# Kernel tuning notes

Hardware: AMD Instinct MI355X
Metric: run time of the kernel (lower is better)

The kernel has to match this reference:

```python
import jax, jax.numpy as jnp
import numpy as np

COST_CLASS, COST_BBOX, COST_GIOU = 1.0, 5.0, 2.0


def _box_area(b):
    return (b[..., 2] - b[..., 0]) * (b[..., 3] - b[..., 1])


def _generalized_box_iou(b1, b2):
    # b1: (B,Q,4), b2: (B,N,4), xyxy -> (B,Q,N)
    a1 = _box_area(b1)[:, :, None]
    a2 = _box_area(b2)[:, None, :]
    lt = jnp.maximum(b1[:, :, None, :2], b2[:, None, :, :2])
    rb = jnp.minimum(b1[:, :, None, 2:], b2[:, None, :, 2:])
    wh = jnp.clip(rb - lt, 0.0)
    inter = wh[..., 0] * wh[..., 1]
    union = a1 + a2 - inter
    iou = inter / union
    lt_c = jnp.minimum(b1[:, :, None, :2], b2[:, None, :, :2])
    rb_c = jnp.maximum(b1[:, :, None, 2:], b2[:, None, :, 2:])
    wh_c = jnp.clip(rb_c - lt_c, 0.0)
    area_c = wh_c[..., 0] * wh_c[..., 1]
    return iou - (area_c - union) / area_c


@jax.jit
def _cost_matrix(pred_logits, pred_boxes, tgt_labels, tgt_boxes):
    B, Q, _ = pred_logits.shape
    N = tgt_labels.shape[1]
    out_prob = jax.nn.softmax(pred_logits, axis=-1)  # (B,Q,C+1)
    idx = jnp.broadcast_to(tgt_labels[:, None, :], (B, Q, N))
    cost_class = -jnp.take_along_axis(out_prob, idx, axis=-1)          # (B,Q,N)
    cost_bbox = jnp.abs(pred_boxes[:, :, None, :] - tgt_boxes[:, None, :, :]).sum(-1)  # L1 cdist
    cost_giou = -_generalized_box_iou(pred_boxes, tgt_boxes)
    return COST_CLASS * cost_class + COST_BBOX * cost_bbox + COST_GIOU * cost_giou


def _lsa(cost):
    """Shortest-augmenting-path Hungarian (Jonker-Volgenant style).
    cost: (n, m) with n <= m. Returns col4row[i] = assigned column of row i.
    Matches scipy.optimize.linear_sum_assignment (minimization)."""
    n, m = cost.shape
    INF = np.inf
    u = np.zeros(n + 1)
    v = np.zeros(m + 1)
    p = np.zeros(m + 1, dtype=np.int64)   # p[j] = row (1-indexed) assigned to col j
    way = np.zeros(m + 1, dtype=np.int64)
    for i in range(1, n + 1):
        p[0] = i
        j0 = 0
        minv = np.full(m + 1, INF)
        used = np.zeros(m + 1, dtype=bool)
        while True:
            used[j0] = True
            i0 = p[j0]
            cur = cost[i0 - 1] - u[i0] - v[1:]
            free = ~used[1:]
            upd = free & (cur < minv[1:])
            minv[1:][upd] = cur[upd]
            way[1:][upd] = j0
            cand = np.where(free, minv[1:], INF)
            j1 = int(np.argmin(cand)) + 1
            delta = cand[j1 - 1]
            uj = np.nonzero(used)[0]
            u[p[uj]] += delta
            v[uj] -= delta
            minv[~used] -= delta
            j0 = j1
            if p[j0] == 0:
                break
        while j0 != 0:
            j1 = way[j0]
            p[j0] = p[j1]
            j0 = j1
    col4row = np.zeros(n, dtype=np.int64)
    for j in range(1, m + 1):
        if p[j] != 0:
            col4row[p[j] - 1] = j - 1
    return col4row


def setup_inputs() -> dict:
    key = jax.random.key(0)
    k1, k2, k3, k4, k5 = jax.random.split(key, 5)
    B, Q, N, C1 = 64, 600, 80, 92

    def make_boxes(kx, ky, shape):
        xy = jax.random.uniform(kx, shape + (2,)) * 0.6
        wh = jax.random.uniform(ky, shape + (2,)) * 0.35 + 0.02
        return jnp.concatenate([xy, xy + wh], axis=-1)  # valid xyxy

    pred_logits = jax.random.normal(k1, (B, Q, C1), dtype=jnp.float32)
    pred_boxes = make_boxes(k2, k3, (B, Q))
    tgt_labels = jax.random.randint(k4, (B, N), 0, 91)
    tgt_boxes = make_boxes(k5, jax.random.fold_in(k5, 1), (B, N))
    return {"pred_logits": pred_logits, "pred_boxes": pred_boxes,
            "tgt_labels": tgt_labels, "tgt_boxes": tgt_boxes}


def reference(pred_logits, pred_boxes, tgt_labels, tgt_boxes):
    # Batched cost-matrix build on device, then host Hungarian per sample
    # (mirrors the original's .cpu().numpy() + scipy linear_sum_assignment).
    C = np.asarray(_cost_matrix(pred_logits, pred_boxes, tgt_labels, tgt_boxes))  # (B,Q,N)
    B, Q, N = C.shape
    rows = np.empty((B, N), dtype=np.int64)
    cols = np.empty((B, N), dtype=np.int64)
    for b in range(B):
        q_of_t = _lsa(C[b].T)              # transpose: N <= Q; query index per target
        order = np.argsort(q_of_t, kind="stable")
        rows[b] = q_of_t[order]            # sorted query (row) indices
        cols[b] = order                    # matching target (col) indices
    return jnp.asarray(rows), jnp.asarray(cols)
```

## Files before the change

### kernel.cpp

```cpp
#include <hip/hip_runtime.h>
#include <math.h>

#define BB 64
#define QQ 600
#define NT 80
#define NC 92
#define SLOTS 10
#define NTILE 10
#define NTHR 256
#define NWAVE 4
#define MAXROUNDS 48
#define SPINCAP (1 << 20)

__global__ __launch_bounds__(256) void matcher_kernel(
    const float* __restrict__ logits,
    const float* __restrict__ pboxes,
    const int*   __restrict__ tlabels,
    const float* __restrict__ tboxes,
    float* __restrict__ cost,
    float* __restrict__ pm1,
    float* __restrict__ pm2,
    int*   __restrict__ pmj,
    int*   __restrict__ done,
    int* __restrict__ rows_out,
    int* __restrict__ cols_out)
{
    __shared__ float tile[64 * 93];
    __shared__ float s_m[64], s_s[64];
    __shared__ float s_pm[4 * 64], s_ps[4 * 64];
    __shared__ float s_tb[NT * 4];
    __shared__ int   s_tl[NT];
    __shared__ double vA[QQ];
    __shared__ double u[NT];
    __shared__ double bidm1[NT], bidm2[NT];
    __shared__ int    bidj[NT], bidver[NT];
    __shared__ int    pA[QQ];
    __shared__ int    verA[QQ];
    __shared__ int    colrow[QQ];
    __shared__ int    assigned[NT];
    __shared__ int    plist[NT];
    __shared__ int    pcnt;
    __shared__ int    wayA[QQ];
    __shared__ int    c4r[NT];
    __shared__ int    djkA[NT];

    const int g   = blockIdx.x;
    const int b   = g / NTILE;
    const int tix = g % NTILE;
    const int tid = threadIdx.x;
    const int qq  = tid & 63;
    const int wv  = tid >> 6;
    const float* C = cost + (size_t)b * NT * QQ;

    {
        const int q0 = tix * 64;
        const int nq = min(64, QQ - q0);
        const float* src = logits + ((size_t)b * QQ + q0) * NC;
        for (int idx = tid; idx < nq * NC; idx += 256) {
            const int r = idx / NC;
            tile[r * 93 + (idx - r * NC)] = src[idx];
        }
        for (int i = tid; i < NT * 4; i += 256) s_tb[i] = tboxes[b * NT * 4 + i];
        for (int i = tid; i < NT;     i += 256) s_tl[i] = tlabels[b * NT + i];
        __syncthreads();

        if (tid < nq) {
            const float* r = &tile[tid * 93];
            float m0 = r[0], m1 = r[1], m2 = r[2], m3 = r[3];
            for (int c = 4; c < NC; c += 4) {
                m0 = fmaxf(m0, r[c]);   m1 = fmaxf(m1, r[c+1]);
                m2 = fmaxf(m2, r[c+2]); m3 = fmaxf(m3, r[c+3]);
            }
            const float m = fmaxf(fmaxf(m0, m1), fmaxf(m2, m3));
            float s0 = 0.f, s1 = 0.f, s2 = 0.f, s3 = 0.f;
            for (int c = 0; c < NC; c += 4) {
                s0 += expf(r[c]   - m); s1 += expf(r[c+1] - m);
                s2 += expf(r[c+2] - m); s3 += expf(r[c+3] - m);
            }
            s_m[tid] = m; s_s[tid] = (s0 + s1) + (s2 + s3);
        }
        __syncthreads();

        const bool valid = qq < nq;
        float px1 = 0.f, py1 = 0.f, px2 = 0.f, py2 = 0.f, pa = 0.f, m = 0.f, s = 1.f;
        if (valid) {
            const float* pb = pboxes + ((size_t)b * QQ + q0 + qq) * 4;
            px1 = pb[0]; py1 = pb[1]; px2 = pb[2]; py2 = pb[3];
            pa  = (px2 - px1) * (py2 - py1);
            m = s_m[qq]; s = s_s[qq];
        }
        float* crow = cost + (size_t)b * NT * QQ + q0 + qq;
        const int q = q0 + qq;

        for (int tt = 0; tt < 20; ++tt) {
            const int t = wv * 20 + tt;
            float costv = INFINITY;
            if (valid) {
                const int lbl = s_tl[t];
                const float cc = -(expf(tile[qq * 93 + lbl] - m) / s);
                const float tx1 = s_tb[t*4+0], ty1 = s_tb[t*4+1];
                const float tx2 = s_tb[t*4+2], ty2 = s_tb[t*4+3];
                const float cb = fabsf(px1-tx1) + fabsf(py1-ty1)
                               + fabsf(px2-tx2) + fabsf(py2-ty2);
                const float ta = (tx2 - tx1) * (ty2 - ty1);
                const float iw = fmaxf(fminf(px2, tx2) - fmaxf(px1, tx1), 0.f);
                const float ih = fmaxf(fminf(py2, ty2) - fmaxf(py1, ty1), 0.f);
                const float inter = iw * ih;
                const float uni   = pa + ta - inter;
                const float iou   = inter / uni;
                const float cw = fmaxf(fmaxf(px2, tx2) - fminf(px1, tx1), 0.f);
                const float ch = fmaxf(fmaxf(py2, ty2) - fminf(py1, ty1), 0.f);
                const float ac = cw * ch;
                const float giou = iou - (ac - uni) / ac;
                costv = (1.0f * cc + 5.0f * cb) + 2.0f * (-giou);
                crow[(size_t)t * QQ] = costv;
            }
            float b1 = costv, b2 = INFINITY; int bj = valid ? q : QQ;
            #pragma unroll
            for (int off = 32; off > 0; off >>= 1) {
                const float o1 = __shfl_xor(b1, off);
                const float o2 = __shfl_xor(b2, off);
                const int   oj = __shfl_xor(bj, off);
                if (o1 < b1 || (o1 == b1 && oj < bj)) {
                    b2 = fminf(b1, o2); b1 = o1; bj = oj;
                } else {
                    b2 = fminf(o1, b2);
                }
            }
            if (qq == 0) {
                const size_t idx = ((size_t)b * NT + t) * NTILE + tix;
                pm1[idx] = b1; pm2[idx] = b2; pmj[idx] = bj;
            }
        }
    }
    __syncthreads();
    if (tid == 0)
        __hip_atomic_fetch_add(&done[b], 1, __ATOMIC_RELEASE, __HIP_MEMORY_SCOPE_AGENT);
    if (tix != 0) return;

    if (tid == 0) {
        int spins = 0;
        while (__hip_atomic_load(&done[b], __ATOMIC_ACQUIRE, __HIP_MEMORY_SCOPE_AGENT) < NTILE) {
            __builtin_amdgcn_s_sleep(8);
            if (++spins > SPINCAP) break;
        }
    }
    __syncthreads();

    for (int c = tid; c < QQ; c += NTHR) { pA[c] = -1; verA[c] = 0; vA[c] = 0.0; }
    if (tid < NT) { assigned[tid] = 0; bidver[tid] = 0; }
    __syncthreads();

    if (tid < NT) {
        const int t = tid;
        const float* p1 = pm1 + ((size_t)b * NT + t) * NTILE;
        const float* p2 = pm2 + ((size_t)b * NT + t) * NTILE;
        const int*   pj = pmj + ((size_t)b * NT + t) * NTILE;
        float m1 = INFINITY, m2 = INFINITY; int j1 = QQ;
        for (int k = 0; k < NTILE; ++k) {
            const float a1 = p1[k], a2 = p2[k];
            const int   aj = pj[k];
            if (a1 < m1) { m2 = fminf(m1, a2); m1 = a1; j1 = aj; }
            else         { m2 = fminf(m2, a1); }
        }
        bidm1[t] = (double)m1; bidm2[t] = (double)m2; bidj[t] = j1;
        u[t] = (double)m1;
    }
    __syncthreads();

    for (int round = 0; round < MAXROUNDS; ++round) {
        for (int c = tid; c < QQ; c += NTHR) colrow[c] = 0x7fffffff;
        if (tid == 0) pcnt = 0;
        __syncthreads();
        if (tid < NT && !assigned[tid]) {
            const int j = bidj[tid];
            if (bidver[tid] == verA[j]) atomicMin(&colrow[j], tid);
        }
        __syncthreads();
        if (tid < NT && !assigned[tid]) {
            const int i = tid, j = bidj[i];
            if (bidver[i] == verA[j] && colrow[j] == i) {
                const double m1 = bidm1[i], m2 = bidm2[i];
                const int prev = pA[j];
                pA[j] = i;
                verA[j] = verA[j] + 1;
                vA[j] -= (m2 - m1);
                u[i] = m2;
                assigned[i] = 1;
                if (prev >= 0) assigned[prev] = 0;
            }
        }
        __syncthreads();
        if (tid < NT && !assigned[tid]) { const int k = atomicAdd(&pcnt, 1); plist[k] = tid; }
        __syncthreads();
        const int np = pcnt;
        if (np == 0) break;
        for (int idx = wv; idx < np; idx += NWAVE) {
            const int i = plist[idx];
            const float* rp = C + (size_t)i * QQ;
            float rowv[SLOTS];
            #pragma unroll
            for (int k = 0; k < SLOTS; ++k) { const int c = qq + 64*k; rowv[k] = (c < QQ) ? rp[c] : 0.f; }
            double m1 = INFINITY, m2 = INFINITY; int j1 = QQ;
            #pragma unroll
            for (int k = 0; k < SLOTS; ++k) {
                const int c = qq + 64 * k;
                if (c < QQ) {
                    const double key = (double)rowv[k] - vA[c];
                    if (key < m1)      { m2 = m1; m1 = key; j1 = c; }
                    else if (key < m2) { m2 = key; }
                }
            }
            #pragma unroll
            for (int off = 32; off > 0; off >>= 1) {
                const double om1 = __shfl_xor(m1, off);
                const int    oj1 = __shfl_xor(j1, off);
                const double om2 = __shfl_xor(m2, off);
                if (om1 < m1 || (om1 == m1 && oj1 < j1)) {
                    m2 = fmin(m1, om2); m1 = om1; j1 = oj1;
                } else {
                    m2 = fmin(om1, m2);
                }
            }
            if (qq == 0) {
                bidm1[i] = m1; bidm2[i] = m2; bidj[i] = j1;
                bidver[i] = verA[j1];
                u[i] = m1;
            }
        }
        __syncthreads();
    }

    if (wv != 0) return;
    const int lane = qq;

    int nd = 0;
    for (int i = 0; i < NT; ++i) {
        if (!assigned[i]) { if (lane == 0) djkA[nd] = i; ++nd; }
    }

    double v_[SLOTS], minv_[SLOTS];
    int p_[SLOTS];
    #pragma unroll
    for (int k = 0; k < SLOTS; ++k) {
        const int c = lane + 64 * k;
        v_[k] = (c < QQ) ? vA[c] : 0.0;
        p_[k] = (c < QQ) ? pA[c] : -1;
    }

    float rowv[SLOTS];
    for (int ii = 0; ii < nd; ++ii) {
        const int i = djkA[ii];
        #pragma unroll
        for (int k = 0; k < SLOTS; ++k) minv_[k] = INFINITY;
        unsigned usedm = 0;
        int j0 = -1;
        double ui0 = u[i];
        {
            const float* rp = C + (size_t)i * QQ;
            #pragma unroll
            for (int k = 0; k < SLOTS; ++k) { const int c = lane + 64*k; rowv[k] = (c < QQ) ? rp[c] : 0.f; }
        }
        int j1, i1;

        for (;;) {
            if (j0 >= 0 && (j0 & 63) == lane) usedm |= 1u << (j0 >> 6);

            double bestv = INFINITY; int bestc = QQ;
            #pragma unroll
            for (int k = 0; k < SLOTS; ++k) {
                const int c = lane + 64 * k;
                if (c < QQ && !((usedm >> k) & 1u)) {
                    const double cur = ((double)rowv[k] - ui0) - v_[k];
                    if (cur < minv_[k]) { minv_[k] = cur; wayA[c] = j0; }
                    if (minv_[k] < bestv) { bestv = minv_[k]; bestc = c; }
                }
            }
            #pragma unroll
            for (int off = 32; off > 0; off >>= 1) {
                const double ov = __shfl_xor(bestv, off);
                const int    oc = __shfl_xor(bestc, off);
                if (ov < bestv || (ov == bestv && oc < bestc)) { bestv = ov; bestc = oc; }
            }
            const double delta = bestv;
            j1 = bestc;

            {
                const int slot = j1 >> 6, lj = j1 & 63;
                int myp = p_[0];
                #pragma unroll
                for (int k = 1; k < SLOTS; ++k) if (slot == k) myp = p_[k];
                i1 = __shfl(myp, lj);
            }

            double ui_next = 0.0;
            float rown[SLOTS];
            if (i1 >= 0) {
                ui_next = u[i1];
                const float* rp = C + (size_t)i1 * QQ;
                #pragma unroll
                for (int k = 0; k < SLOTS; ++k) { const int c = lane + 64*k; rown[k] = (c < QQ) ? rp[c] : 0.f; }
            }

            #pragma unroll
            for (int k = 0; k < SLOTS; ++k) {
                const int c = lane + 64 * k;
                if (c < QQ) {
                    if ((usedm >> k) & 1u) { v_[k] -= delta; u[p_[k]] += delta; }
                    else                     minv_[k] -= delta;
                }
            }
            if (lane == 0) u[i] += delta;

            j0 = j1;
            if (i1 < 0) break;
            ui0 = ui_next;
            #pragma unroll
            for (int k = 0; k < SLOTS; ++k) rowv[k] = rown[k];
        }

        if (lane == 0) {
            int jj = j1;
            while (jj >= 0) {
                const int pr = wayA[jj];
                pA[jj] = (pr < 0) ? i : pA[pr];
                jj = pr;
            }
        }
        #pragma unroll
        for (int k = 0; k < SLOTS; ++k) {
            const int c = lane + 64 * k;
            p_[k] = (c < QQ) ? pA[c] : -1;
        }
    }

    #pragma unroll
    for (int k = 0; k < SLOTS; ++k) {
        const int c = lane + 64 * k;
        if (c < QQ) { const int t = pA[c]; if (t >= 0) c4r[t] = c; }
    }
    for (int t = lane; t < NT; t += 64) {
        const int c = c4r[t];
        int rank = 0;
        for (int t2 = 0; t2 < NT; ++t2) rank += (c4r[t2] < c) ? 1 : 0;
        rows_out[b * NT + rank] = c;
        cols_out[b * NT + rank] = t;
    }
}

extern "C" void kernel_launch(void* const* d_in, const int* in_sizes, int n_in,
                              void* d_out, int out_size, void* d_ws, size_t ws_size,
                              hipStream_t stream) {
    (void)in_sizes; (void)n_in; (void)out_size; (void)ws_size;
    const float* logits  = (const float*)d_in[0];
    const float* pboxes  = (const float*)d_in[1];
    const int*   tlabels = (const int*)d_in[2];
    const float* tboxes  = (const float*)d_in[3];
    float* cost = (float*)d_ws;
    float* pm1  = cost + (size_t)BB * NT * QQ;
    float* pm2  = pm1  + (size_t)BB * NT * NTILE;
    int*   pmj  = (int*)(pm2 + (size_t)BB * NT * NTILE);
    int*   done = pmj + (size_t)BB * NT * NTILE;
    int*   out  = (int*)d_out;

    hipMemsetAsync(done, 0, BB * sizeof(int), stream);
    matcher_kernel<<<dim3(BB * NTILE), NTHR, 0, stream>>>(
        logits, pboxes, tlabels, tboxes, cost, pm1, pm2, pmj, done,
        out, out + BB * NT);
}
```

Measured before the change: 133.0 us.

## Cache softmax exps in tile and trim barriers in auction rounds

The softmax pass now writes exp(x-m) back into the shared tile, so the cost loop only divides instead of recomputing expf per target. The auction loop is restructured to use two barriers per round instead of four: colrow and pcnt are reset at the end of the previous round, and the unassigned list is built during the assignment step. A stall detector ends the auction early if the unassigned count stops shrinking for three rounds, leaving the remainder to the exact JV fallback. This could add more fallback work, and it relies on plist holding each unassigned row exactly once.

Result: slower. 150.6 us (+13.2%).

```diff
diff --git a/kernel.cpp b/kernel.cpp
--- a/kernel.cpp
+++ b/kernel.cpp
@@ -27,7 +27,6 @@
 {
     __shared__ float tile[64 * 93];
     __shared__ float s_m[64], s_s[64];
-    __shared__ float s_pm[4 * 64], s_ps[4 * 64];
     __shared__ float s_tb[NT * 4];
     __shared__ int   s_tl[NT];
     __shared__ double vA[QQ];
@@ -65,7 +64,7 @@
         __syncthreads();
 
         if (tid < nq) {
-            const float* r = &tile[tid * 93];
+            float* r = &tile[tid * 93];
             float m0 = r[0], m1 = r[1], m2 = r[2], m3 = r[3];
             for (int c = 4; c < NC; c += 4) {
                 m0 = fmaxf(m0, r[c]);   m1 = fmaxf(m1, r[c+1]);
@@ -74,20 +73,22 @@
             const float m = fmaxf(fmaxf(m0, m1), fmaxf(m2, m3));
             float s0 = 0.f, s1 = 0.f, s2 = 0.f, s3 = 0.f;
             for (int c = 0; c < NC; c += 4) {
-                s0 += expf(r[c]   - m); s1 += expf(r[c+1] - m);
-                s2 += expf(r[c+2] - m); s3 += expf(r[c+3] - m);
+                const float e0 = expf(r[c]   - m); r[c]   = e0; s0 += e0;
+                const float e1 = expf(r[c+1] - m); r[c+1] = e1; s1 += e1;
+                const float e2 = expf(r[c+2] - m); r[c+2] = e2; s2 += e2;
+                const float e3 = expf(r[c+3] - m); r[c+3] = e3; s3 += e3;
             }
             s_m[tid] = m; s_s[tid] = (s0 + s1) + (s2 + s3);
         }
         __syncthreads();
 
         const bool valid = qq < nq;
-        float px1 = 0.f, py1 = 0.f, px2 = 0.f, py2 = 0.f, pa = 0.f, m = 0.f, s = 1.f;
+        float px1 = 0.f, py1 = 0.f, px2 = 0.f, py2 = 0.f, pa = 0.f, s = 1.f;
         if (valid) {
             const float* pb = pboxes + ((size_t)b * QQ + q0 + qq) * 4;
             px1 = pb[0]; py1 = pb[1]; px2 = pb[2]; py2 = pb[3];
             pa  = (px2 - px1) * (py2 - py1);
-            m = s_m[qq]; s = s_s[qq];
+            s   = s_s[qq];
         }
         float* crow = cost + (size_t)b * NT * QQ + q0 + qq;
         const int q = q0 + qq;
@@ -97,7 +98,7 @@
             float costv = INFINITY;
             if (valid) {
                 const int lbl = s_tl[t];
-                const float cc = -(expf(tile[qq * 93 + lbl] - m) / s);
+                const float cc = -(tile[qq * 93 + lbl] / s);
                 const float tx1 = s_tb[t*4+0], ty1 = s_tb[t*4+1];
                 const float tx2 = s_tb[t*4+2], ty2 = s_tb[t*4+3];
                 const float cb = fabsf(px1-tx1) + fabsf(py1-ty1)
@@ -147,8 +148,9 @@
     }
     __syncthreads();
 
-    for (int c = tid; c < QQ; c += NTHR) { pA[c] = -1; verA[c] = 0; vA[c] = 0.0; }
+    for (int c = tid; c < QQ; c += NTHR) { pA[c] = -1; verA[c] = 0; vA[c] = 0.0; colrow[c] = 0x7fffffff; }
     if (tid < NT) { assigned[tid] = 0; bidver[tid] = 0; }
+    if (tid == 0) pcnt = 0;
     __syncthreads();
 
     if (tid < NT) {
@@ -168,68 +170,77 @@
     }
     __syncthreads();
 
-    for (int round = 0; round < MAXROUNDS; ++round) {
-        for (int c = tid; c < QQ; c += NTHR) colrow[c] = 0x7fffffff;
-        if (tid == 0) pcnt = 0;
-        __syncthreads();
-        if (tid < NT && !assigned[tid]) {
-            const int j = bidj[tid];
-            if (bidver[tid] == verA[j]) atomicMin(&colrow[j], tid);
-        }
-        __syncthreads();
-        if (tid < NT && !assigned[tid]) {
-            const int i = tid, j = bidj[i];
-            if (bidver[i] == verA[j] && colrow[j] == i) {
-                const double m1 = bidm1[i], m2 = bidm2[i];
-                const int prev = pA[j];
-                pA[j] = i;
-                verA[j] = verA[j] + 1;
-                vA[j] -= (m2 - m1);
-                u[i] = m2;
-                assigned[i] = 1;
-                if (prev >= 0) assigned[prev] = 0;
-            }
-        }
-        __syncthreads();
-        if (tid < NT && !assigned[tid]) { const int k = atomicAdd(&pcnt, 1); plist[k] = tid; }
-        __syncthreads();
-        const int np = pcnt;
-        if (np == 0) break;
-        for (int idx = wv; idx < np; idx += NWAVE) {
-            const int i = plist[idx];
-            const float* rp = C + (size_t)i * QQ;
-            float rowv[SLOTS];
-            #pragma unroll
-            for (int k = 0; k < SLOTS; ++k) { const int c = qq + 64*k; rowv[k] = (c < QQ) ? rp[c] : 0.f; }
-            double m1 = INFINITY, m2 = INFINITY; int j1 = QQ;
-            #pragma unroll
-            for (int k = 0; k < SLOTS; ++k) {
-                const int c = qq + 64 * k;
-                if (c < QQ) {
-                    const double key = (double)rowv[k] - vA[c];
-                    if (key < m1)      { m2 = m1; m1 = key; j1 = c; }
-                    else if (key < m2) { m2 = key; }
-                }
-            }
-            #pragma unroll
-            for (int off = 32; off > 0; off >>= 1) {
-                const double om1 = __shfl_xor(m1, off);
-                const int    oj1 = __shfl_xor(j1, off);
-                const double om2 = __shfl_xor(m2, off);
-                if (om1 < m1 || (om1 == m1 && oj1 < j1)) {
-                    m2 = fmin(m1, om2); m1 = om1; j1 = oj1;
+    {
+        int np_prev = 0x7fffffff, stall = 0;
+        for (int round = 0; round < MAXROUNDS; ++round) {
+            const bool act = (tid < NT) && (assigned[tid] == 0);
+            const int  i   = tid;
+            int jbid = -1; bool fresh = false;
+            if (act) {
+                jbid  = bidj[i];
+                fresh = (bidver[i] == verA[jbid]);
+                if (fresh) atomicMin(&colrow[jbid], i);
+            }
+            __syncthreads();
+            if (act) {
+                if (fresh && colrow[jbid] == i) {
+                    const double m1 = bidm1[i], m2 = bidm2[i];
+                    const int prev = pA[jbid];
+                    pA[jbid] = i;
+                    verA[jbid] = verA[jbid] + 1;
+                    vA[jbid] -= (m2 - m1);
+                    u[i] = m2;
+                    assigned[i] = 1;
+                    if (prev >= 0) { assigned[prev] = 0; plist[atomicAdd(&pcnt, 1)] = prev; }
                 } else {
-                    m2 = fmin(om1, m2);
-                }
-            }
-            if (qq == 0) {
-                bidm1[i] = m1; bidm2[i] = m2; bidj[i] = j1;
-                bidver[i] = verA[j1];
-                u[i] = m1;
-            }
-        }
-        __syncthreads();
-    }
+                    plist[atomicAdd(&pcnt, 1)] = i;
+                }
+            }
+            __syncthreads();
+            const int np = pcnt;
+            if (np == 0) break;
+            if (np >= np_prev) { if (++stall >= 3) break; }
+            else stall = 0;
+            np_prev = np;
+            for (int idx = wv; idx < np; idx += NWAVE) {
+                const int ri = plist[idx];
+                const float* rp = C + (size_t)ri * QQ;
+                float rowv[SLOTS];
+                #pragma unroll
+                for (int k = 0; k < SLOTS; ++k) { const int c = qq + 64*k; rowv[k] = (c < QQ) ? rp[c] : 0.f; }
+                double m1 = INFINITY, m2 = INFINITY; int j1 = QQ;
+                #pragma unroll
+                for (int k = 0; k < SLOTS; ++k) {
+                    const int c = qq + 64 * k;
+                    if (c < QQ) {
+                        const double key = (double)rowv[k] - vA[c];
+                        if (key < m1)      { m2 = m1; m1 = key; j1 = c; }
+                        else if (key < m2) { m2 = key; }
+                    }
+                }
+                #pragma unroll
+                for (int off = 32; off > 0; off >>= 1) {
+                    const double om1 = __shfl_xor(m1, off);
+                    const int    oj1 = __shfl_xor(j1, off);
+                    const double om2 = __shfl_xor(m2, off);
+                    if (om1 < m1 || (om1 == m1 && oj1 < j1)) {
+                        m2 = fmin(m1, om2); m1 = om1; j1 = oj1;
+                    } else {
+                        m2 = fmin(om1, m2);
+                    }
+                }
+                if (qq == 0) {
+                    bidm1[ri] = m1; bidm2[ri] = m2; bidj[ri] = j1;
+                    bidver[ri] = verA[j1];
+                    u[ri] = m1;
+                }
+            }
+            for (int c = tid; c < QQ; c += NTHR) colrow[c] = 0x7fffffff;
+            if (tid == 0) pcnt = 0;
+            __syncthreads();
+        }
+    }
+    __syncthreads();
 
     if (wv != 0) return;
     const int lane = qq;
```
